# Kernel tuning notes

Measured on AMD Instinct MI355X. Metric: run time of the kernel, lower is better.

## Reference

```python
import jax, jax.numpy as jnp
import numpy as np
import math

B, H, S, DK = 4, 16, 2048, 64
NEG = -1e9

def setup_inputs() -> dict:
    key = jax.random.key(0)
    kq, kk, kv, km = jax.random.split(key, 4)
    Q = jax.random.normal(kq, (B, H, S, DK), dtype=jnp.float32)
    K = jax.random.normal(kk, (B, H, S, DK), dtype=jnp.float32)
    V = jax.random.normal(kv, (B, H, S, DK), dtype=jnp.float32)
    mask = jax.random.randint(km, (1, 1, S, S), 0, 2, dtype=jnp.int32)
    return {"Q": Q, "K": K, "V": V, "mask": mask}

def reference(Q, K, V, mask):
    d_k = K.shape[-1]
    # [B,H,S,S] scores = Q K^T / sqrt(d_k)
    scores = jnp.einsum('bhqd,bhkd->bhqk', Q, K) / math.sqrt(d_k)
    scores = jnp.where(mask == 0, jnp.float32(NEG), scores)
    probs = jax.nn.softmax(scores, axis=-1)
    out = jnp.einsum('bhqk,bhkd->bhqd', probs, V)
    return (out, probs)
```

## Files before the change

### kernel.cpp

```cpp
#include <hip/hip_runtime.h>
#include <hip/hip_bf16.h>

#define S_LEN 2048
#define NT    32
#define DKC   64
#define NEGV  (-1e9f)
#define C_SC  0.18033688011112042f

typedef __attribute__((ext_vector_type(8))) short short8v;
typedef __attribute__((ext_vector_type(4))) float f32x4;

__device__ __forceinline__ short f2bf(float f){
  unsigned u = __builtin_bit_cast(unsigned, f);
  u += 0x7fffu + ((u >> 16) & 1u);
  return (short)(u >> 16);
}

__device__ __forceinline__ int swz(int row, int col){
  return (row * 64 + col) ^ ((row & 7) << 3);
}

__device__ __forceinline__ void xcd_decode(int p, int& bh, int& qt){
  const int xcd = p & 7;
  const int n   = p >> 3;
  bh = ((n >> 5) << 3) | xcd;
  qt = n & 31;
}

__device__ __forceinline__ void stage_rows_bf16(short* dst, const float* src, int tid){
  const int r  = tid >> 2;
  const int c0 = (tid & 3) * 16;
  const float* p = src + (size_t)r * DKC + c0;
  float4 a0 = *(const float4*)(p);
  float4 a1 = *(const float4*)(p + 4);
  float4 a2 = *(const float4*)(p + 8);
  float4 a3 = *(const float4*)(p + 12);
  short8v s0, s1;
  s0[0]=f2bf(a0.x); s0[1]=f2bf(a0.y); s0[2]=f2bf(a0.z); s0[3]=f2bf(a0.w);
  s0[4]=f2bf(a1.x); s0[5]=f2bf(a1.y); s0[6]=f2bf(a1.z); s0[7]=f2bf(a1.w);
  s1[0]=f2bf(a2.x); s1[1]=f2bf(a2.y); s1[2]=f2bf(a2.z); s1[3]=f2bf(a2.w);
  s1[4]=f2bf(a3.x); s1[5]=f2bf(a3.y); s1[6]=f2bf(a3.z); s1[7]=f2bf(a3.w);
  *(short8v*)&dst[swz(r, c0)]     = s0;
  *(short8v*)&dst[swz(r, c0 + 8)] = s1;
}

__device__ __forceinline__ void stage_vT_bf16(short* dst, const float* src, int tid){
  const int k  = tid >> 4;
  const int d0 = (tid & 15) * 4;
  #pragma unroll
  for (int i = 0; i < 4; ++i){
    const int kk = k + 16 * i;
    const float4 v = *(const float4*)(src + (size_t)kk * DKC + d0);
    dst[swz(d0 + 0, kk)] = f2bf(v.x);
    dst[swz(d0 + 1, kk)] = f2bf(v.y);
    dst[swz(d0 + 2, kk)] = f2bf(v.z);
    dst[swz(d0 + 3, kk)] = f2bf(v.w);
  }
}

__global__ void maskpack_kernel(const int* __restrict__ mask, unsigned long long* __restrict__ bits){
  const int w    = blockIdx.x * 4 + (threadIdx.x >> 6);
  const int lane = threadIdx.x & 63;
  for (int i = 0; i < 64; ++i){
    const size_t word = (size_t)w * 64 + i;
    const int v = mask[word * 64 + lane];
    const unsigned long long b = __ballot(v != 0);
    if (lane == 0) bits[word] = b;
  }
}

__global__ __launch_bounds__(256) void kvq_convert(
    const float* __restrict__ Kg, const float* __restrict__ Vg, const float* __restrict__ Qg,
    short* __restrict__ Kimg, short* __restrict__ Vimg, short* __restrict__ Qimg){
  __shared__ float Vf[64][65];
  const int tid = threadIdx.x;
  int bh, t;
  xcd_decode(blockIdx.x, bh, t);
  const size_t tile = (size_t)bh * NT + t;
  const float* Kb = Kg + tile * (64 * 64);
  const float* Vb = Vg + tile * (64 * 64);
  const float* Qb = Qg + tile * (64 * 64);
  short* Ki = Kimg + tile * 4096;
  short* Vi = Vimg + tile * 4096;
  short* Qi = Qimg + tile * 4096;
  {
    const int r = tid >> 2, c0 = (tid & 3) * 16;
    const float* p = Kb + (size_t)r * 64 + c0;
    float4 a0 = *(const float4*)(p);
    float4 a1 = *(const float4*)(p + 4);
    float4 a2 = *(const float4*)(p + 8);
    float4 a3 = *(const float4*)(p + 12);
    short8v s0, s1;
    s0[0]=f2bf(a0.x); s0[1]=f2bf(a0.y); s0[2]=f2bf(a0.z); s0[3]=f2bf(a0.w);
    s0[4]=f2bf(a1.x); s0[5]=f2bf(a1.y); s0[6]=f2bf(a1.z); s0[7]=f2bf(a1.w);
    s1[0]=f2bf(a2.x); s1[1]=f2bf(a2.y); s1[2]=f2bf(a2.z); s1[3]=f2bf(a2.w);
    s1[4]=f2bf(a3.x); s1[5]=f2bf(a3.y); s1[6]=f2bf(a3.z); s1[7]=f2bf(a3.w);
    *(short8v*)&Ki[swz(r, c0)]     = s0;
    *(short8v*)&Ki[swz(r, c0 + 8)] = s1;

    const float* q = Qb + (size_t)r * 64 + c0;
    float4 b0 = *(const float4*)(q);
    float4 b1 = *(const float4*)(q + 4);
    float4 b2 = *(const float4*)(q + 8);
    float4 b3 = *(const float4*)(q + 12);
    short8v t0, t1;
    t0[0]=f2bf(b0.x); t0[1]=f2bf(b0.y); t0[2]=f2bf(b0.z); t0[3]=f2bf(b0.w);
    t0[4]=f2bf(b1.x); t0[5]=f2bf(b1.y); t0[6]=f2bf(b1.z); t0[7]=f2bf(b1.w);
    t1[0]=f2bf(b2.x); t1[1]=f2bf(b2.y); t1[2]=f2bf(b2.z); t1[3]=f2bf(b2.w);
    t1[4]=f2bf(b3.x); t1[5]=f2bf(b3.y); t1[6]=f2bf(b3.z); t1[7]=f2bf(b3.w);
    *(short8v*)&Qi[r * 64 + c0]     = t0;
    *(short8v*)&Qi[r * 64 + c0 + 8] = t1;
  }
  {
    const int k = tid >> 2, c0 = (tid & 3) * 16;
    const float* p = Vb + (size_t)k * 64 + c0;
    float4 a0 = *(const float4*)(p);
    float4 a1 = *(const float4*)(p + 4);
    float4 a2 = *(const float4*)(p + 8);
    float4 a3 = *(const float4*)(p + 12);
    Vf[k][c0+0]=a0.x; Vf[k][c0+1]=a0.y; Vf[k][c0+2]=a0.z; Vf[k][c0+3]=a0.w;
    Vf[k][c0+4]=a1.x; Vf[k][c0+5]=a1.y; Vf[k][c0+6]=a1.z; Vf[k][c0+7]=a1.w;
    Vf[k][c0+8]=a2.x; Vf[k][c0+9]=a2.y; Vf[k][c0+10]=a2.z; Vf[k][c0+11]=a2.w;
    Vf[k][c0+12]=a3.x; Vf[k][c0+13]=a3.y; Vf[k][c0+14]=a3.z; Vf[k][c0+15]=a3.w;
  }
  __syncthreads();
  {
    const int d = tid >> 2, k0 = (tid & 3) * 16;
    short8v s0, s1;
    #pragma unroll
    for (int i = 0; i < 8; ++i) s0[i] = f2bf(Vf[k0 + i][d]);
    #pragma unroll
    for (int i = 0; i < 8; ++i) s1[i] = f2bf(Vf[k0 + 8 + i][d]);
    *(short8v*)&Vi[swz(d, k0)]     = s0;
    *(short8v*)&Vi[swz(d, k0 + 8)] = s1;
  }
}

__device__ __forceinline__ void loadK(short8v (&kf)[8], const short* Kt, int ll, int lh){
  #pragma unroll
  for (int kt = 0; kt < 4; ++kt){
    kf[kt*2+0] = *(const short8v*)(Kt + swz(kt * 16 + ll, lh * 8));
    kf[kt*2+1] = *(const short8v*)(Kt + swz(kt * 16 + ll, 32 + lh * 8));
  }
}

__device__ __forceinline__ float tile_sum(const short8v (&kf)[8], const short8v (&qf)[2],
                                          unsigned long long wb, int lh){
  float s0 = 0.f, s1 = 0.f;
  #pragma unroll
  for (int kt = 0; kt < 4; ++kt){
    f32x4 a = (f32x4){0.f, 0.f, 0.f, 0.f};
    a = __builtin_amdgcn_mfma_f32_16x16x32_bf16(kf[kt*2+0], qf[0], a, 0, 0, 0);
    a = __builtin_amdgcn_mfma_f32_16x16x32_bf16(kf[kt*2+1], qf[1], a, 0, 0, 0);
    #pragma unroll
    for (int j = 0; j < 4; ++j){
      const int bi = kt * 16 + lh * 4 + j;
      const float arg = ((wb >> bi) & 1ull) ? a[j] * C_SC : NEGV;
      if (j & 1) s1 += exp2f(arg); else s0 += exp2f(arg);
    }
  }
  return s0 + s1;
}

__global__ __launch_bounds__(256) void pass_sum(
    const short* __restrict__ Qimg, const unsigned long long* __restrict__ bitsg,
    const short* __restrict__ Kimg, float* __restrict__ lnl)
{
  const int tid  = threadIdx.x;
  const int wid  = tid >> 6;
  const int lane = tid & 63;
  const int lh   = lane >> 4;
  const int ll   = lane & 15;

  int bh, qt;
  xcd_decode(blockIdx.x, bh, qt);
  const int qrow = qt * 64 + wid * 16 + ll;

  const short* Qib = Qimg + (size_t)bh * S_LEN * 64;
  const short* Kib = Kimg + (size_t)bh * NT * 4096;

  short8v qf[2];
  qf[0] = *(const short8v*)(Qib + (size_t)qrow * 64 + lh * 8);
  qf[1] = *(const short8v*)(Qib + (size_t)qrow * 64 + 32 + lh * 8);

  float sum = 0.f;
  short8v ka[8], kb[8];
  loadK(ka, Kib, ll, lh);
  for (int tt = 0; tt < NT; tt += 2){
    loadK(kb, Kib + (size_t)(tt + 1) * 4096, ll, lh);
    sum += tile_sum(ka, qf, bitsg[(size_t)qrow * NT + tt], lh);
    const int nx = (tt + 2 < NT) ? tt + 2 : NT - 1;
    loadK(ka, Kib + (size_t)nx * 4096, ll, lh);
    sum += tile_sum(kb, qf, bitsg[(size_t)qrow * NT + tt + 1], lh);
  }
  sum += __shfl_xor(sum, 16, 64);
  sum += __shfl_xor(sum, 32, 64);
  if (lh == 0) lnl[bh * S_LEN + qrow] = __log2f(sum);
}

__global__ __launch_bounds__(256) void pass_out(
    const short* __restrict__ Qimg, const unsigned long long* __restrict__ bitsg,
    const short* __restrict__ Kimg, const short* __restrict__ Vimg,
    const float* __restrict__ lnl, float* __restrict__ outg, float* __restrict__ probsg)
{
  __shared__ __align__(16) short Pl[4096];

  const int tid  = threadIdx.x;
  const int wid  = tid >> 6;
  const int lane = tid & 63;
  const int lh   = lane >> 4;
  const int ll   = lane & 15;

  int bh, qt;
  xcd_decode(blockIdx.x, bh, qt);
  const int qrow = qt * 64 + wid * 16 + ll;

  const short* Qib = Qimg + (size_t)bh * S_LEN * 64;
  const short* Kib = Kimg + (size_t)bh * NT * 4096;
  const short* Vib = Vimg + (size_t)bh * NT * 4096;
  float* outb   = outg   + (size_t)bh * S_LEN * DKC;
  float* probsb = probsg + (size_t)bh * S_LEN * S_LEN;

  short8v qf[2];
  qf[0] = *(const short8v*)(Qib + (size_t)qrow * 64 + lh * 8);
  qf[1] = *(const short8v*)(Qib + (size_t)qrow * 64 + 32 + lh * 8);
  const float rlog = lnl[bh * S_LEN + qrow];

  f32x4 o[4];
  #pragma unroll
  for (int dt = 0; dt < 4; ++dt) o[dt] = (f32x4){0.f, 0.f, 0.f, 0.f};

  for (int t = 0; t < NT; ++t){
    const unsigned long long wb = bitsg[(size_t)qrow * NT + t];
    const short* Vt_ = Vib + (size_t)t * 4096;
    const short* Kt_ = Kib + (size_t)t * 4096;

    short8v vf[8];
    #pragma unroll
    for (int k32 = 0; k32 < 2; ++k32)
      #pragma unroll
      for (int dt = 0; dt < 4; ++dt)
        vf[k32*4+dt] = *(const short8v*)(Vt_ + swz(dt * 16 + ll, k32 * 32 + lh * 8));

    short8v kf[8];
    loadK(kf, Kt_, ll, lh);

    f32x4 acc[4];
    #pragma unroll
    for (int kt = 0; kt < 4; ++kt){
      f32x4 a = (f32x4){0.f, 0.f, 0.f, 0.f};
      a = __builtin_amdgcn_mfma_f32_16x16x32_bf16(kf[kt*2+0], qf[0], a, 0, 0, 0);
      a = __builtin_amdgcn_mfma_f32_16x16x32_bf16(kf[kt*2+1], qf[1], a, 0, 0, 0);
      acc[kt] = a;
    }

    #pragma unroll
    for (int kt = 0; kt < 4; ++kt){
      float p[4];
      #pragma unroll
      for (int j = 0; j < 4; ++j){
        const int bi = kt * 16 + lh * 4 + j;
        const float arg = ((wb >> bi) & 1ull) ? fmaf(acc[kt][j], C_SC, -rlog) : NEGV;
        p[j] = exp2f(arg);
      }
      f32x4 pv; pv[0]=p[0]; pv[1]=p[1]; pv[2]=p[2]; pv[3]=p[3];
      __builtin_nontemporal_store(pv, (f32x4*)&probsb[(size_t)qrow * S_LEN + t * 64 + kt * 16 + lh * 4]);
      short4 ps; ps.x=f2bf(p[0]); ps.y=f2bf(p[1]); ps.z=f2bf(p[2]); ps.w=f2bf(p[3]);
      *(short4*)&Pl[wid * 1024 + swz(ll, kt * 16 + lh * 4)] = ps;
    }

    #pragma unroll
    for (int k32 = 0; k32 < 2; ++k32){
      const short8v pf = *(const short8v*)&Pl[wid * 1024 + swz(ll, k32 * 32 + lh * 8)];
      #pragma unroll
      for (int dt = 0; dt < 4; ++dt)
        o[dt] = __builtin_amdgcn_mfma_f32_16x16x32_bf16(pf, vf[k32*4+dt], o[dt], 0, 0, 0);
    }
  }

  #pragma unroll
  for (int dt = 0; dt < 4; ++dt)
    #pragma unroll
    for (int j = 0; j < 4; ++j)
      __builtin_nontemporal_store(o[dt][j], &outb[(size_t)(qt * 64 + wid * 16 + lh * 4 + j) * DKC + dt * 16 + ll]);
}

template<int BITS>
__global__ __launch_bounds__(256) void attn_fb(
    const float* __restrict__ Qg, const float* __restrict__ Kg, const float* __restrict__ Vg,
    const int* __restrict__ maskg, const unsigned long long* __restrict__ bitsg,
    float* __restrict__ outg, float* __restrict__ probsg)
{
  __shared__ __align__(16) short Kl[4096];
  __shared__ __align__(16) short Vt[4096];
  __shared__ __align__(16) short Pl[4096];

  const int tid  = threadIdx.x;
  const int wid  = tid >> 6;
  const int lane = tid & 63;
  const int lh   = lane >> 4;
  const int ll   = lane & 15;

  const int qt    = blockIdx.x & 31;
  const int bh    = blockIdx.x >> 5;
  const int qbase = qt * 64;
  const int qrow  = qbase + wid * 16 + ll;

  const float* Qb = Qg + (size_t)bh * S_LEN * DKC;
  const float* Kb = Kg + (size_t)bh * S_LEN * DKC;
  const float* Vb = Vg + (size_t)bh * S_LEN * DKC;
  float* outb   = outg   + (size_t)bh * S_LEN * DKC;
  float* probsb = probsg + (size_t)bh * S_LEN * S_LEN;

  short8v qf[2];
  #pragma unroll
  for (int h = 0; h < 2; ++h){
    const float4 a = *(const float4*)(Qb + (size_t)qrow * DKC + h * 32 + lh * 8);
    const float4 b = *(const float4*)(Qb + (size_t)qrow * DKC + h * 32 + lh * 8 + 4);
    short8v t;
    t[0]=f2bf(a.x); t[1]=f2bf(a.y); t[2]=f2bf(a.z); t[3]=f2bf(a.w);
    t[4]=f2bf(b.x); t[5]=f2bf(b.y); t[6]=f2bf(b.z); t[7]=f2bf(b.w);
    qf[h] = t;
  }

  float sum = 0.f;
  for (int t = 0; t < NT; ++t){
    __syncthreads();
    stage_rows_bf16(Kl, Kb + (size_t)t * 64 * DKC, tid);
    __syncthreads();
    unsigned long long wb = 0;
    if constexpr (BITS) wb = bitsg[(size_t)qrow * NT + t];
    #pragma unroll
    for (int kt = 0; kt < 4; ++kt){
      const short8v kf0 = *(const short8v*)&Kl[swz(kt * 16 + ll, lh * 8)];
      const short8v kf1 = *(const short8v*)&Kl[swz(kt * 16 + ll, 32 + lh * 8)];
      f32x4 a = (f32x4){0.f, 0.f, 0.f, 0.f};
      a = __builtin_amdgcn_mfma_f32_16x16x32_bf16(kf0, qf[0], a, 0, 0, 0);
      a = __builtin_amdgcn_mfma_f32_16x16x32_bf16(kf1, qf[1], a, 0, 0, 0);
      #pragma unroll
      for (int j = 0; j < 4; ++j){
        const int bi = kt * 16 + lh * 4 + j;
        int keep;
        if constexpr (BITS) keep = (int)((wb >> bi) & 1ull);
        else                keep = maskg[(size_t)qrow * S_LEN + t * 64 + bi] != 0;
        sum += exp2f(keep ? a[j] * C_SC : NEGV);
      }
    }
  }
  sum += __shfl_xor(sum, 16, 64);
  sum += __shfl_xor(sum, 32, 64);
  const float rlog = __log2f(sum);

  f32x4 o[4];
  #pragma unroll
  for (int dt = 0; dt < 4; ++dt) o[dt] = (f32x4){0.f, 0.f, 0.f, 0.f};

  for (int t = 0; t < NT; ++t){
    __syncthreads();
    stage_rows_bf16(Kl, Kb + (size_t)t * 64 * DKC, tid);
    stage_vT_bf16 (Vt, Vb + (size_t)t * 64 * DKC, tid);
    __syncthreads();
    f32x4 acc[4];
    #pragma unroll
    for (int kt = 0; kt < 4; ++kt){
      const short8v kf0 = *(const short8v*)&Kl[swz(kt * 16 + ll, lh * 8)];
      const short8v kf1 = *(const short8v*)&Kl[swz(kt * 16 + ll, 32 + lh * 8)];
      f32x4 a = (f32x4){0.f, 0.f, 0.f, 0.f};
      a = __builtin_amdgcn_mfma_f32_16x16x32_bf16(kf0, qf[0], a, 0, 0, 0);
      a = __builtin_amdgcn_mfma_f32_16x16x32_bf16(kf1, qf[1], a, 0, 0, 0);
      acc[kt] = a;
    }
    unsigned long long wb = 0;
    if constexpr (BITS) wb = bitsg[(size_t)qrow * NT + t];
    #pragma unroll
    for (int kt = 0; kt < 4; ++kt){
      float p[4];
      #pragma unroll
      for (int j = 0; j < 4; ++j){
        const int bi = kt * 16 + lh * 4 + j;
        int keep;
        if constexpr (BITS) keep = (int)((wb >> bi) & 1ull);
        else                keep = maskg[(size_t)qrow * S_LEN + t * 64 + bi] != 0;
        p[j] = exp2f(keep ? fmaf(acc[kt][j], C_SC, -rlog) : NEGV);
      }
      f32x4 pv; pv[0]=p[0]; pv[1]=p[1]; pv[2]=p[2]; pv[3]=p[3];
      __builtin_nontemporal_store(pv, (f32x4*)&probsb[(size_t)qrow * S_LEN + t * 64 + kt * 16 + lh * 4]);
      short4 ps; ps.x=f2bf(p[0]); ps.y=f2bf(p[1]); ps.z=f2bf(p[2]); ps.w=f2bf(p[3]);
      *(short4*)&Pl[wid * 1024 + swz(ll, kt * 16 + lh * 4)] = ps;
    }
    asm volatile("s_waitcnt lgkmcnt(0)" ::: "memory");
    __builtin_amdgcn_sched_barrier(0);
    #pragma unroll
    for (int k32 = 0; k32 < 2; ++k32){
      const short8v pf = *(const short8v*)&Pl[wid * 1024 + swz(ll, k32 * 32 + lh * 8)];
      #pragma unroll
      for (int dt = 0; dt < 4; ++dt){
        const short8v vf = *(const short8v*)&Vt[swz(dt * 16 + ll, k32 * 32 + lh * 8)];
        o[dt] = __builtin_amdgcn_mfma_f32_16x16x32_bf16(pf, vf, o[dt], 0, 0, 0);
      }
    }
  }

  #pragma unroll
  for (int dt = 0; dt < 4; ++dt)
    #pragma unroll
    for (int j = 0; j < 4; ++j)
      __builtin_nontemporal_store(o[dt][j], &outb[(size_t)(qbase + wid * 16 + lh * 4 + j) * DKC + dt * 16 + ll]);
}

extern "C" void kernel_launch(void* const* d_in, const int* in_sizes, int n_in,
                              void* d_out, int out_size, void* d_ws, size_t ws_size,
                              hipStream_t stream) {
  const float* Q    = (const float*)d_in[0];
  const float* K    = (const float*)d_in[1];
  const float* V    = (const float*)d_in[2];
  const int*   mask = (const int*)d_in[3];

  float* out   = (float*)d_out;
  float* probs = out + (size_t)4 * 16 * 2048 * 64;

  const size_t bitsB = (size_t)S_LEN * S_LEN / 8;
  const size_t imgB  = (size_t)64 * NT * 4096 * 2;
  const size_t lnlB  = (size_t)64 * S_LEN * 4;
  unsigned long long* bits = (unsigned long long*)d_ws;
  short* Kimg = (short*)((char*)d_ws + bitsB);
  short* Vimg = (short*)((char*)d_ws + bitsB + imgB);
  short* Qimg = (short*)((char*)d_ws + bitsB + 2 * imgB);
  float* lnl  = (float*)((char*)d_ws + bitsB + 3 * imgB);

  int mode;
  if      (ws_size >= bitsB + 3 * imgB + lnlB) mode = 2;
  else if (ws_size >= bitsB)                   mode = 1;
  else                                         mode = 0;

  if (mode >= 1) maskpack_kernel<<<256, 256, 0, stream>>>(mask, bits);

  if (mode == 2){
    kvq_convert<<<64 * NT, 256, 0, stream>>>(K, V, Q, Kimg, Vimg, Qimg);
    pass_sum<<<64 * 32, 256, 0, stream>>>(Qimg, bits, Kimg, lnl);
    pass_out<<<64 * 32, 256, 0, stream>>>(Qimg, bits, Kimg, Vimg, lnl, out, probs);
  } else if (mode == 1){
    attn_fb<1><<<64 * 32, 256, 0, stream>>>(Q, K, V, mask, bits, out, probs);
  } else {
    attn_fb<0><<<64 * 32, 256, 0, stream>>>(Q, K, V, mask, bits, out, probs);
  }
}
```

Measured before the change: 475.8 us.

## Fuse softmax-sum and output passes into one kernel, drop lnl buffer

Merges the row-sum pass and the probs/output pass into a single kernel, so each block computes the row log-sum and then immediately makes the second sweep. This removes one launch and the lnl round trip, and the reversed second sweep reuses the K tiles most recently read, which are likely still in cache. It also swaps the masking select for a multiply by the mask bit, adds a launch-bounds occupancy hint, and splits the V fragment loads to cut register pressure. The cost is a longer per-block critical path and possible register-pressure limits from the hint.

```diff
diff --git a/kernel.cpp b/kernel.cpp
--- a/kernel.cpp
+++ b/kernel.cpp
@@ -144,28 +144,13 @@
   }
 }
 
-__device__ __forceinline__ float tile_sum(const short8v (&kf)[8], const short8v (&qf)[2],
-                                          unsigned long long wb, int lh){
-  float s0 = 0.f, s1 = 0.f;
-  #pragma unroll
-  for (int kt = 0; kt < 4; ++kt){
-    f32x4 a = (f32x4){0.f, 0.f, 0.f, 0.f};
-    a = __builtin_amdgcn_mfma_f32_16x16x32_bf16(kf[kt*2+0], qf[0], a, 0, 0, 0);
-    a = __builtin_amdgcn_mfma_f32_16x16x32_bf16(kf[kt*2+1], qf[1], a, 0, 0, 0);
-    #pragma unroll
-    for (int j = 0; j < 4; ++j){
-      const int bi = kt * 16 + lh * 4 + j;
-      const float arg = ((wb >> bi) & 1ull) ? a[j] * C_SC : NEGV;
-      if (j & 1) s1 += exp2f(arg); else s0 += exp2f(arg);
-    }
-  }
-  return s0 + s1;
-}
-
-__global__ __launch_bounds__(256) void pass_sum(
+__global__ __launch_bounds__(256, 4) void attn_ws(
     const short* __restrict__ Qimg, const unsigned long long* __restrict__ bitsg,
-    const short* __restrict__ Kimg, float* __restrict__ lnl)
+    const short* __restrict__ Kimg, const short* __restrict__ Vimg,
+    float* __restrict__ outg, float* __restrict__ probsg)
 {
+  __shared__ __align__(16) short Pl[4096];
+
   const int tid  = threadIdx.x;
   const int wid  = tid >> 6;
   const int lane = tid & 63;
@@ -178,72 +163,53 @@
 
   const short* Qib = Qimg + (size_t)bh * S_LEN * 64;
   const short* Kib = Kimg + (size_t)bh * NT * 4096;
+  const short* Vib = Vimg + (size_t)bh * NT * 4096;
+  float* outb   = outg   + (size_t)bh * S_LEN * DKC;
+  float* probsb = probsg + (size_t)bh * S_LEN * S_LEN;
 
   short8v qf[2];
   qf[0] = *(const short8v*)(Qib + (size_t)qrow * 64 + lh * 8);
   qf[1] = *(const short8v*)(Qib + (size_t)qrow * 64 + 32 + lh * 8);
 
   float sum = 0.f;
-  short8v ka[8], kb[8];
-  loadK(ka, Kib, ll, lh);
-  for (int tt = 0; tt < NT; tt += 2){
-    loadK(kb, Kib + (size_t)(tt + 1) * 4096, ll, lh);
-    sum += tile_sum(ka, qf, bitsg[(size_t)qrow * NT + tt], lh);
-    const int nx = (tt + 2 < NT) ? tt + 2 : NT - 1;
-    loadK(ka, Kib + (size_t)nx * 4096, ll, lh);
-    sum += tile_sum(kb, qf, bitsg[(size_t)qrow * NT + tt + 1], lh);
+  #pragma unroll 2
+  for (int t = 0; t < NT; ++t){
+    short8v kf[8];
+    loadK(kf, Kib + (size_t)t * 4096, ll, lh);
+    const unsigned long long wb = bitsg[(size_t)qrow * NT + t];
+    #pragma unroll
+    for (int kt = 0; kt < 4; ++kt){
+      f32x4 a = (f32x4){0.f, 0.f, 0.f, 0.f};
+      a = __builtin_amdgcn_mfma_f32_16x16x32_bf16(kf[kt*2+0], qf[0], a, 0, 0, 0);
+      a = __builtin_amdgcn_mfma_f32_16x16x32_bf16(kf[kt*2+1], qf[1], a, 0, 0, 0);
+      #pragma unroll
+      for (int j = 0; j < 4; ++j){
+        const int bi = kt * 16 + lh * 4 + j;
+        const float mf = (float)((wb >> bi) & 1ull);
+        sum += exp2f(a[j] * C_SC) * mf;
+      }
+    }
   }
   sum += __shfl_xor(sum, 16, 64);
   sum += __shfl_xor(sum, 32, 64);
-  if (lh == 0) lnl[bh * S_LEN + qrow] = __log2f(sum);
-}
-
-__global__ __launch_bounds__(256) void pass_out(
-    const short* __restrict__ Qimg, const unsigned long long* __restrict__ bitsg,
-    const short* __restrict__ Kimg, const short* __restrict__ Vimg,
-    const float* __restrict__ lnl, float* __restrict__ outg, float* __restrict__ probsg)
-{
-  __shared__ __align__(16) short Pl[4096];
-
-  const int tid  = threadIdx.x;
-  const int wid  = tid >> 6;
-  const int lane = tid & 63;
-  const int lh   = lane >> 4;
-  const int ll   = lane & 15;
-
-  int bh, qt;
-  xcd_decode(blockIdx.x, bh, qt);
-  const int qrow = qt * 64 + wid * 16 + ll;
-
-  const short* Qib = Qimg + (size_t)bh * S_LEN * 64;
-  const short* Kib = Kimg + (size_t)bh * NT * 4096;
-  const short* Vib = Vimg + (size_t)bh * NT * 4096;
-  float* outb   = outg   + (size_t)bh * S_LEN * DKC;
-  float* probsb = probsg + (size_t)bh * S_LEN * S_LEN;
-
-  short8v qf[2];
-  qf[0] = *(const short8v*)(Qib + (size_t)qrow * 64 + lh * 8);
-  qf[1] = *(const short8v*)(Qib + (size_t)qrow * 64 + 32 + lh * 8);
-  const float rlog = lnl[bh * S_LEN + qrow];
+  const float rlog = __log2f(sum);
 
   f32x4 o[4];
   #pragma unroll
   for (int dt = 0; dt < 4; ++dt) o[dt] = (f32x4){0.f, 0.f, 0.f, 0.f};
 
-  for (int t = 0; t < NT; ++t){
+  for (int t = NT - 1; t >= 0; --t){
     const unsigned long long wb = bitsg[(size_t)qrow * NT + t];
     const short* Vt_ = Vib + (size_t)t * 4096;
     const short* Kt_ = Kib + (size_t)t * 4096;
 
-    short8v vf[8];
-    #pragma unroll
-    for (int k32 = 0; k32 < 2; ++k32)
-      #pragma unroll
-      for (int dt = 0; dt < 4; ++dt)
-        vf[k32*4+dt] = *(const short8v*)(Vt_ + swz(dt * 16 + ll, k32 * 32 + lh * 8));
-
     short8v kf[8];
     loadK(kf, Kt_, ll, lh);
+
+    short8v vf0[4];
+    #pragma unroll
+    for (int dt = 0; dt < 4; ++dt)
+      vf0[dt] = *(const short8v*)(Vt_ + swz(dt * 16 + ll, lh * 8));
 
     f32x4 acc[4];
     #pragma unroll
@@ -260,8 +226,8 @@
       #pragma unroll
       for (int j = 0; j < 4; ++j){
         const int bi = kt * 16 + lh * 4 + j;
-        const float arg = ((wb >> bi) & 1ull) ? fmaf(acc[kt][j], C_SC, -rlog) : NEGV;
-        p[j] = exp2f(arg);
+        const float mf = (float)((wb >> bi) & 1ull);
+        p[j] = exp2f(fmaf(acc[kt][j], C_SC, -rlog)) * mf;
       }
       f32x4 pv; pv[0]=p[0]; pv[1]=p[1]; pv[2]=p[2]; pv[3]=p[3];
       __builtin_nontemporal_store(pv, (f32x4*)&probsb[(size_t)qrow * S_LEN + t * 64 + kt * 16 + lh * 4]);
@@ -269,12 +235,20 @@
       *(short4*)&Pl[wid * 1024 + swz(ll, kt * 16 + lh * 4)] = ps;
     }
 
-    #pragma unroll
-    for (int k32 = 0; k32 < 2; ++k32){
-      const short8v pf = *(const short8v*)&Pl[wid * 1024 + swz(ll, k32 * 32 + lh * 8)];
+    short8v vf1[4];
+    #pragma unroll
+    for (int dt = 0; dt < 4; ++dt)
+      vf1[dt] = *(const short8v*)(Vt_ + swz(dt * 16 + ll, 32 + lh * 8));
+
+    {
+      const short8v pf0 = *(const short8v*)&Pl[wid * 1024 + swz(ll, lh * 8)];
       #pragma unroll
       for (int dt = 0; dt < 4; ++dt)
-        o[dt] = __builtin_amdgcn_mfma_f32_16x16x32_bf16(pf, vf[k32*4+dt], o[dt], 0, 0, 0);
+        o[dt] = __builtin_amdgcn_mfma_f32_16x16x32_bf16(pf0, vf0[dt], o[dt], 0, 0, 0);
+      const short8v pf1 = *(const short8v*)&Pl[wid * 1024 + swz(ll, 32 + lh * 8)];
+      #pragma unroll
+      for (int dt = 0; dt < 4; ++dt)
+        o[dt] = __builtin_amdgcn_mfma_f32_16x16x32_bf16(pf1, vf1[dt], o[dt], 0, 0, 0);
     }
   }
 
@@ -421,24 +395,21 @@
 
   const size_t bitsB = (size_t)S_LEN * S_LEN / 8;
   const size_t imgB  = (size_t)64 * NT * 4096 * 2;
-  const size_t lnlB  = (size_t)64 * S_LEN * 4;
   unsigned long long* bits = (unsigned long long*)d_ws;
   short* Kimg = (short*)((char*)d_ws + bitsB);
   short* Vimg = (short*)((char*)d_ws + bitsB + imgB);
   short* Qimg = (short*)((char*)d_ws + bitsB + 2 * imgB);
-  float* lnl  = (float*)((char*)d_ws + bitsB + 3 * imgB);
 
   int mode;
-  if      (ws_size >= bitsB + 3 * imgB + lnlB) mode = 2;
-  else if (ws_size >= bitsB)                   mode = 1;
-  else                                         mode = 0;
+  if      (ws_size >= bitsB + 3 * imgB) mode = 2;
+  else if (ws_size >= bitsB)            mode = 1;
+  else                                  mode = 0;
 
   if (mode >= 1) maskpack_kernel<<<256, 256, 0, stream>>>(mask, bits);
 
   if (mode == 2){
     kvq_convert<<<64 * NT, 256, 0, stream>>>(K, V, Q, Kimg, Vimg, Qimg);
-    pass_sum<<<64 * 32, 256, 0, stream>>>(Qimg, bits, Kimg, lnl);
-    pass_out<<<64 * 32, 256, 0, stream>>>(Qimg, bits, Kimg, Vimg, lnl, out, probs);
+    attn_ws<<<64 * 32, 256, 0, stream>>>(Qimg, bits, Kimg, Vimg, out, probs);
   } else if (mode == 1){
     attn_fb<1><<<64 * 32, 256, 0, stream>>>(Q, K, V, mask, bits, out, probs);
   } else {
```

Result: no change. 483.6 us (+1.6%).

## Fuse mask packing into convert kernel and restructure score loops

Applied to the files above, without the earlier changes.

Folds the mask bit-packing into the kvq_convert kernel, which removes one kernel launch in the main path. pass_sum drops its manual double-buffered K prefetch and uses a plain unrolled loop. Masking changes from a select against -1e9 to multiplying exp2 by a 0/1 float. pass_out is split into two half-tiles so fewer K/V fragments are live in registers at once. bf16 packing of probabilities now uses a cheaper round-half-up instead of round-to-nearest-even. The multiply-mask form can give inf*0 = NaN if an unmasked score overflows exp2, and it changes rounding slightly.

```diff
diff --git a/kernel.cpp b/kernel.cpp
--- a/kernel.cpp
+++ b/kernel.cpp
@@ -9,11 +9,18 @@
 
 typedef __attribute__((ext_vector_type(8))) short short8v;
 typedef __attribute__((ext_vector_type(4))) float f32x4;
+typedef __attribute__((ext_vector_type(2))) unsigned uint2v;
 
 __device__ __forceinline__ short f2bf(float f){
   unsigned u = __builtin_bit_cast(unsigned, f);
   u += 0x7fffu + ((u >> 16) & 1u);
   return (short)(u >> 16);
+}
+
+__device__ __forceinline__ unsigned packbf(float a, float b){
+  const unsigned ua = __builtin_bit_cast(unsigned, a) + 0x8000u;
+  const unsigned ub = __builtin_bit_cast(unsigned, b) + 0x8000u;
+  return (ua >> 16) | (ub & 0xFFFF0000u);
 }
 
 __device__ __forceinline__ int swz(int row, int col){
@@ -71,9 +78,12 @@
 
 __global__ __launch_bounds__(256) void kvq_convert(
     const float* __restrict__ Kg, const float* __restrict__ Vg, const float* __restrict__ Qg,
+    const int* __restrict__ mask, unsigned long long* __restrict__ bits,
     short* __restrict__ Kimg, short* __restrict__ Vimg, short* __restrict__ Qimg){
   __shared__ float Vf[64][65];
-  const int tid = threadIdx.x;
+  const int tid  = threadIdx.x;
+  const int wid  = tid >> 6;
+  const int lane = tid & 63;
   int bh, t;
   xcd_decode(blockIdx.x, bh, t);
   const size_t tile = (size_t)bh * NT + t;
@@ -83,6 +93,18 @@
   short* Ki = Kimg + tile * 4096;
   short* Vi = Vimg + tile * 4096;
   short* Qi = Qimg + tile * 4096;
+
+  {
+    const int gw = blockIdx.x * 4 + wid;
+    #pragma unroll
+    for (int i = 0; i < 8; ++i){
+      const size_t word = (size_t)gw * 8 + i;
+      const int v = mask[word * 64 + lane];
+      const unsigned long long b = __ballot(v != 0);
+      if (lane == 0) bits[word] = b;
+    }
+  }
+
   {
     const int r = tid >> 2, c0 = (tid & 3) * 16;
     const float* p = Kb + (size_t)r * 64 + c0;
@@ -136,32 +158,6 @@
   }
 }
 
-__device__ __forceinline__ void loadK(short8v (&kf)[8], const short* Kt, int ll, int lh){
-  #pragma unroll
-  for (int kt = 0; kt < 4; ++kt){
-    kf[kt*2+0] = *(const short8v*)(Kt + swz(kt * 16 + ll, lh * 8));
-    kf[kt*2+1] = *(const short8v*)(Kt + swz(kt * 16 + ll, 32 + lh * 8));
-  }
-}
-
-__device__ __forceinline__ float tile_sum(const short8v (&kf)[8], const short8v (&qf)[2],
-                                          unsigned long long wb, int lh){
-  float s0 = 0.f, s1 = 0.f;
-  #pragma unroll
-  for (int kt = 0; kt < 4; ++kt){
-    f32x4 a = (f32x4){0.f, 0.f, 0.f, 0.f};
-    a = __builtin_amdgcn_mfma_f32_16x16x32_bf16(kf[kt*2+0], qf[0], a, 0, 0, 0);
-    a = __builtin_amdgcn_mfma_f32_16x16x32_bf16(kf[kt*2+1], qf[1], a, 0, 0, 0);
-    #pragma unroll
-    for (int j = 0; j < 4; ++j){
-      const int bi = kt * 16 + lh * 4 + j;
-      const float arg = ((wb >> bi) & 1ull) ? a[j] * C_SC : NEGV;
-      if (j & 1) s1 += exp2f(arg); else s0 += exp2f(arg);
-    }
-  }
-  return s0 + s1;
-}
-
 __global__ __launch_bounds__(256) void pass_sum(
     const short* __restrict__ Qimg, const unsigned long long* __restrict__ bitsg,
     const short* __restrict__ Kimg, float* __restrict__ lnl)
@@ -184,14 +180,28 @@
   qf[1] = *(const short8v*)(Qib + (size_t)qrow * 64 + 32 + lh * 8);
 
   float sum = 0.f;
-  short8v ka[8], kb[8];
-  loadK(ka, Kib, ll, lh);
-  for (int tt = 0; tt < NT; tt += 2){
-    loadK(kb, Kib + (size_t)(tt + 1) * 4096, ll, lh);
-    sum += tile_sum(ka, qf, bitsg[(size_t)qrow * NT + tt], lh);
-    const int nx = (tt + 2 < NT) ? tt + 2 : NT - 1;
-    loadK(ka, Kib + (size_t)nx * 4096, ll, lh);
-    sum += tile_sum(kb, qf, bitsg[(size_t)qrow * NT + tt + 1], lh);
+  #pragma unroll 2
+  for (int t = 0; t < NT; ++t){
+    const short* Kt_ = Kib + (size_t)t * 4096;
+    const unsigned long long wb = bitsg[(size_t)qrow * NT + t];
+    short8v kf[8];
+    #pragma unroll
+    for (int kt = 0; kt < 4; ++kt){
+      kf[kt*2+0] = *(const short8v*)(Kt_ + swz(kt * 16 + ll, lh * 8));
+      kf[kt*2+1] = *(const short8v*)(Kt_ + swz(kt * 16 + ll, 32 + lh * 8));
+    }
+    #pragma unroll
+    for (int kt = 0; kt < 4; ++kt){
+      f32x4 a = (f32x4){0.f, 0.f, 0.f, 0.f};
+      a = __builtin_amdgcn_mfma_f32_16x16x32_bf16(kf[kt*2+0], qf[0], a, 0, 0, 0);
+      a = __builtin_amdgcn_mfma_f32_16x16x32_bf16(kf[kt*2+1], qf[1], a, 0, 0, 0);
+      #pragma unroll
+      for (int j = 0; j < 4; ++j){
+        const int bi = kt * 16 + lh * 4 + j;
+        const float mf = (float)((wb >> bi) & 1ull);
+        sum += exp2f(a[j] * C_SC) * mf;
+      }
+    }
   }
   sum += __shfl_xor(sum, 16, 64);
   sum += __shfl_xor(sum, 32, 64);
@@ -230,51 +240,55 @@
   #pragma unroll
   for (int dt = 0; dt < 4; ++dt) o[dt] = (f32x4){0.f, 0.f, 0.f, 0.f};
 
+  short* Plw = &Pl[wid * 1024];
+
   for (int t = 0; t < NT; ++t){
     const unsigned long long wb = bitsg[(size_t)qrow * NT + t];
+    const short* Kt_ = Kib + (size_t)t * 4096;
     const short* Vt_ = Vib + (size_t)t * 4096;
-    const short* Kt_ = Kib + (size_t)t * 4096;
-
-    short8v vf[8];
-    #pragma unroll
-    for (int k32 = 0; k32 < 2; ++k32)
+
+    #pragma unroll
+    for (int h = 0; h < 2; ++h){
+      short8v kf[4], vf[4];
+      #pragma unroll
+      for (int q = 0; q < 2; ++q){
+        const int kt = h * 2 + q;
+        kf[q*2+0] = *(const short8v*)(Kt_ + swz(kt * 16 + ll, lh * 8));
+        kf[q*2+1] = *(const short8v*)(Kt_ + swz(kt * 16 + ll, 32 + lh * 8));
+      }
       #pragma unroll
       for (int dt = 0; dt < 4; ++dt)
-        vf[k32*4+dt] = *(const short8v*)(Vt_ + swz(dt * 16 + ll, k32 * 32 + lh * 8));
-
-    short8v kf[8];
-    loadK(kf, Kt_, ll, lh);
-
-    f32x4 acc[4];
-    #pragma unroll
-    for (int kt = 0; kt < 4; ++kt){
-      f32x4 a = (f32x4){0.f, 0.f, 0.f, 0.f};
-      a = __builtin_amdgcn_mfma_f32_16x16x32_bf16(kf[kt*2+0], qf[0], a, 0, 0, 0);
-      a = __builtin_amdgcn_mfma_f32_16x16x32_bf16(kf[kt*2+1], qf[1], a, 0, 0, 0);
-      acc[kt] = a;
-    }
-
-    #pragma unroll
-    for (int kt = 0; kt < 4; ++kt){
-      float p[4];
-      #pragma unroll
-      for (int j = 0; j < 4; ++j){
-        const int bi = kt * 16 + lh * 4 + j;
-        const float arg = ((wb >> bi) & 1ull) ? fmaf(acc[kt][j], C_SC, -rlog) : NEGV;
-        p[j] = exp2f(arg);
-      }
-      f32x4 pv; pv[0]=p[0]; pv[1]=p[1]; pv[2]=p[2]; pv[3]=p[3];
-      __builtin_nontemporal_store(pv, (f32x4*)&probsb[(size_t)qrow * S_LEN + t * 64 + kt * 16 + lh * 4]);
-      short4 ps; ps.x=f2bf(p[0]); ps.y=f2bf(p[1]); ps.z=f2bf(p[2]); ps.w=f2bf(p[3]);
-      *(short4*)&Pl[wid * 1024 + swz(ll, kt * 16 + lh * 4)] = ps;
-    }
-
-    #pragma unroll
-    for (int k32 = 0; k32 < 2; ++k32){
-      const short8v pf = *(const short8v*)&Pl[wid * 1024 + swz(ll, k32 * 32 + lh * 8)];
+        vf[dt] = *(const short8v*)(Vt_ + swz(dt * 16 + ll, h * 32 + lh * 8));
+
+      f32x4 acc[2];
+      #pragma unroll
+      for (int q = 0; q < 2; ++q){
+        f32x4 a = (f32x4){0.f, 0.f, 0.f, 0.f};
+        a = __builtin_amdgcn_mfma_f32_16x16x32_bf16(kf[q*2+0], qf[0], a, 0, 0, 0);
+        a = __builtin_amdgcn_mfma_f32_16x16x32_bf16(kf[q*2+1], qf[1], a, 0, 0, 0);
+        acc[q] = a;
+      }
+
+      #pragma unroll
+      for (int q = 0; q < 2; ++q){
+        const int kt = h * 2 + q;
+        float p[4];
+        #pragma unroll
+        for (int j = 0; j < 4; ++j){
+          const int bi = kt * 16 + lh * 4 + j;
+          const float mf = (float)((wb >> bi) & 1ull);
+          p[j] = exp2f(fmaf(acc[q][j], C_SC, -rlog)) * mf;
+        }
+        f32x4 pv; pv[0]=p[0]; pv[1]=p[1]; pv[2]=p[2]; pv[3]=p[3];
+        __builtin_nontemporal_store(pv, (f32x4*)&probsb[(size_t)qrow * S_LEN + t * 64 + kt * 16 + lh * 4]);
+        uint2v pk; pk[0] = packbf(p[0], p[1]); pk[1] = packbf(p[2], p[3]);
+        *(uint2v*)&Plw[swz(ll, kt * 16 + lh * 4)] = pk;
+      }
+
+      const short8v pf = *(const short8v*)&Plw[swz(ll, h * 32 + lh * 8)];
       #pragma unroll
       for (int dt = 0; dt < 4; ++dt)
-        o[dt] = __builtin_amdgcn_mfma_f32_16x16x32_bf16(pf, vf[k32*4+dt], o[dt], 0, 0, 0);
+        o[dt] = __builtin_amdgcn_mfma_f32_16x16x32_bf16(pf, vf[dt], o[dt], 0, 0, 0);
     }
   }
 
@@ -433,13 +447,12 @@
   else if (ws_size >= bitsB)                   mode = 1;
   else                                         mode = 0;
 
-  if (mode >= 1) maskpack_kernel<<<256, 256, 0, stream>>>(mask, bits);
-
   if (mode == 2){
-    kvq_convert<<<64 * NT, 256, 0, stream>>>(K, V, Q, Kimg, Vimg, Qimg);
+    kvq_convert<<<64 * NT, 256, 0, stream>>>(K, V, Q, mask, bits, Kimg, Vimg, Qimg);
     pass_sum<<<64 * 32, 256, 0, stream>>>(Qimg, bits, Kimg, lnl);
     pass_out<<<64 * 32, 256, 0, stream>>>(Qimg, bits, Kimg, Vimg, lnl, out, probs);
   } else if (mode == 1){
+    maskpack_kernel<<<256, 256, 0, stream>>>(mask, bits);
     attn_fb<1><<<64 * 32, 256, 0, stream>>>(Q, K, V, mask, bits, out, probs);
   } else {
     attn_fb<0><<<64 * 32, 256, 0, stream>>>(Q, K, V, mask, bits, out, probs);
```

Result: no change. 468.5 us (-1.5%).
